# Kernel tuning notes

Measured on AMD Instinct MI355X. Metric: run time of the kernel, lower is better.

## Reference

```python
import jax, jax.numpy as jnp
import numpy as np

N_NODES = 100000
N_EDGES = 1600000
D_IN = 128
D_HID = 128
N_LAYERS = 3


def setup_inputs() -> dict:
    key = jax.random.key(0)
    k1, k2, k3, k4 = jax.random.split(key, 4)
    x = jax.random.normal(k1, (N_NODES, D_IN), dtype=jnp.float32)
    edge_index = jax.random.randint(k2, (2, N_EDGES), 0, N_NODES, dtype=jnp.int64)
    # Glorot-ish scale for stability across 3 layers
    Ws = jax.random.normal(k3, (N_LAYERS, D_IN, D_HID), dtype=jnp.float32) * (1.0 / np.sqrt(D_IN))
    bs = jax.random.normal(k4, (N_LAYERS, D_HID), dtype=jnp.float32) * 0.01
    return {"x": x, "edge_index": edge_index, "Ws": Ws, "bs": bs}


def _gcn_conv(x, row, col, deg_inv_sqrt, W, b, n_nodes):
    # Linear transform first (PyG GCNConv), then gather-normalize-scatter.
    h = x @ W                                        # [N, D]
    norm = deg_inv_sqrt[row] * deg_inv_sqrt[col]     # [E+N] (self-loops included)
    msg = h[row] * norm[:, None]                     # gather + scale, [E+N, D]
    out = jax.ops.segment_sum(msg, col, num_segments=n_nodes)  # scatter-add
    return out + b


def reference(x, edge_index, Ws, bs):
    n = x.shape[0]
    # add self-loops once (same for every layer)
    loop = jnp.arange(n, dtype=edge_index.dtype)
    row = jnp.concatenate([edge_index[0], loop])
    col = jnp.concatenate([edge_index[1], loop])
    # symmetric normalization: deg over target nodes (incl. self-loops)
    deg = jax.ops.segment_sum(jnp.ones_like(col, dtype=x.dtype), col, num_segments=n)
    deg_inv_sqrt = jnp.where(deg > 0, jax.lax.rsqrt(jnp.maximum(deg, 1.0)), 0.0)
    h = x
    for i in range(Ws.shape[0]):
        h = jax.nn.relu(_gcn_conv(h, row, col, deg_inv_sqrt, Ws[i], bs[i], n))
    return h
```

## Files before the change

kernel.cpp:

```cpp
#include <hip/hip_runtime.h>
#include <hip/hip_bf16.h>

#define NN 100000
#define NE 1600000
#define DD 128
#define NBUK 196
#define F1_BLOCKS 256
#define F3_BLOCKS 256

typedef unsigned short ushort_t;
typedef unsigned int uint_t;
typedef __attribute__((ext_vector_type(8))) short bf16x8;
typedef __attribute__((ext_vector_type(4))) float f32x4;

__device__ __forceinline__ ushort_t bf16rne(float f) {
    uint_t u = __float_as_uint(f);
    u += 0x7FFF + ((u >> 16) & 1);
    return (ushort_t)(u >> 16);
}
__device__ __forceinline__ float bfLo(uint_t u) { return __uint_as_float(u << 16); }
__device__ __forceinline__ float bfHi(uint_t u) { return __uint_as_float(u & 0xFFFF0000u); }


__global__ __launch_bounds__(256) void f1_bucket_count(const int* __restrict__ col,
                                                       int* __restrict__ bukCount) {
    __shared__ int hist[NBUK];
    for (int t = threadIdx.x; t < NBUK; t += 256) hist[t] = 0;
    __syncthreads();
    const int epb = (NE + F1_BLOCKS - 1) / F1_BLOCKS;
    const int e0 = blockIdx.x * epb;
    const int e1 = min(e0 + epb, NE);
    for (int e = e0 + threadIdx.x; e < e1; e += 256)
        atomicAdd(&hist[col[e] >> 9], 1);
    __syncthreads();
    for (int t = threadIdx.x; t < NBUK; t += 256)
        if (hist[t]) atomicAdd(&bukCount[t], hist[t]);
}

__global__ void f2_bucket_scan(const int* __restrict__ bukCount,
                               int* __restrict__ bukBase,
                               int* __restrict__ bukCursor,
                               int* __restrict__ offsets) {
    __shared__ int s[256];
    const int t = threadIdx.x;
    int v = (t < NBUK) ? bukCount[t] : 0;
    s[t] = v;
    __syncthreads();
    for (int off = 1; off < 256; off <<= 1) {
        int tmp = (t >= off) ? s[t - off] : 0;
        __syncthreads();
        s[t] += tmp;
        __syncthreads();
    }
    int excl = s[t] - v;
    if (t < NBUK) { bukBase[t] = excl; bukCursor[t] = excl; }
    if (t == 255) { bukBase[NBUK] = s[255]; offsets[NN] = s[255]; }
}

__global__ __launch_bounds__(256) void f3_scatter(const int* __restrict__ row,
                                                  const int* __restrict__ col,
                                                  int* __restrict__ bukCursor,
                                                  int* __restrict__ ebuf) {
    __shared__ int hist[4][NBUK];
    __shared__ int base[4][NBUK];
    const int t = threadIdx.x;
    const int w = t >> 6;
    const int lane = t & 63;
    for (int i = t; i < 4 * NBUK; i += 256) (&hist[0][0])[i] = 0;
    __syncthreads();
    const int epb = (NE + F3_BLOCKS - 1) / F3_BLOCKS;
    const int e0 = blockIdx.x * epb;
    const int e1 = min(e0 + epb, NE);
    const int wepb = (e1 - e0 + 3) >> 2;
    const int we0 = e0 + w * wepb;
    const int we1 = min(we0 + wepb, e1);
    for (int e = we0 + lane; e < we1; e += 64)
        atomicAdd(&hist[w][col[e] >> 9], 1);
    __syncthreads();
    if (t < NBUK) {
        int h0 = hist[0][t], h1 = hist[1][t], h2 = hist[2][t], h3 = hist[3][t];
        int tot = h0 + h1 + h2 + h3;
        int g = tot ? atomicAdd(&bukCursor[t], tot) : 0;
        base[0][t] = g; base[1][t] = g + h0;
        base[2][t] = g + h0 + h1; base[3][t] = g + h0 + h1 + h2;
        hist[0][t] = 0; hist[1][t] = 0; hist[2][t] = 0; hist[3][t] = 0;
    }
    __syncthreads();
    for (int e = we0 + lane; e < we1; e += 64) {
        int c = col[e];
        int b = c >> 9;
        int r = atomicAdd(&hist[w][b], 1);
        ebuf[base[w][b] + r] = (row[e] << 9) | (c & 511);
    }
}

__global__ __launch_bounds__(256) void f4_finalize(const int* __restrict__ ebuf,
                                                   const int* __restrict__ bukBase,
                                                   int* __restrict__ offsets,
                                                   float* __restrict__ dis,
                                                   int* __restrict__ csr_src) {
    __shared__ int cnt[512];
    __shared__ int cur[512];
    __shared__ int s[256];
    const int t = threadIdx.x;
    const int colBase = blockIdx.x << 9;
    const int ncols = min(512, NN - colBase);
    cnt[t] = 0; cnt[t + 256] = 0;
    __syncthreads();
    const int eb0 = bukBase[blockIdx.x];
    const int eb1 = bukBase[blockIdx.x + 1];
    for (int e = eb0 + t; e < eb1; e += 256)
        atomicAdd(&cnt[ebuf[e] & 511], 1);
    __syncthreads();
    const int c0 = cnt[2 * t], c1 = cnt[2 * t + 1];
    const int psum = c0 + c1;
    s[t] = psum;
    __syncthreads();
    for (int off = 1; off < 256; off <<= 1) {
        int tmp = (t >= off) ? s[t - off] : 0;
        __syncthreads();
        s[t] += tmp;
        __syncthreads();
    }
    const int exclPair = s[t] - psum;
    const int g0 = eb0 + exclPair;
    const int g1 = g0 + c0;
    cur[2 * t] = g0; cur[2 * t + 1] = g1;
    if (2 * t < ncols)     { offsets[colBase + 2 * t]     = g0; dis[colBase + 2 * t]     = rsqrtf((float)(c0 + 1)); }
    if (2 * t + 1 < ncols) { offsets[colBase + 2 * t + 1] = g1; dis[colBase + 2 * t + 1] = rsqrtf((float)(c1 + 1)); }
    __syncthreads();
    for (int e = eb0 + t; e < eb1; e += 256) {
        int pc = ebuf[e];
        int p = atomicAdd(&cur[pc & 511], 1);
        csr_src[p] = pc >> 9;
    }
}


__global__ __launch_bounds__(256) void wt_kernel(const float* __restrict__ Ws,
                                                 ushort_t* __restrict__ wT) {
    int idx = blockIdx.x * 256 + threadIdx.x;
    if (idx >= 3 * 128 * 16) return;
    int l = idx >> 11;
    int r = idx & 2047;
    int c = r >> 4;
    int kc = r & 15;
    const float* w = Ws + l * 16384;
    ushort_t tmp[8];
#pragma unroll
    for (int e = 0; e < 8; ++e)
        tmp[e] = bf16rne(w[(kc * 8 + e) * 128 + c]);
    *(uint4*)&wT[(size_t)l * 16384 + c * 128 + kc * 8] = *(uint4*)tmp;
}


template<bool XF32>
__global__ __launch_bounds__(256) void gemm_mfma(const void* __restrict__ Xv,
                                                 const ushort_t* __restrict__ wT,
                                                 const float* __restrict__ dis,
                                                 ushort_t* __restrict__ Y) {
    __shared__ short wlds[128 * 136];
    {
        const uint4* src = (const uint4*)wT;
        int t = threadIdx.x;
#pragma unroll
        for (int i = 0; i < 8; ++i) {
            int idx = i * 256 + t;
            int rowc = idx >> 4;
            int kc = idx & 15;
            uint4 v = src[idx];
            *(uint4*)&wlds[rowc * 136 + kc * 8] = v;
        }
    }
    __syncthreads();

    const int wave = threadIdx.x >> 6;
    const int lane = threadIdx.x & 63;
    const int m = lane & 15;
    const int kg = lane >> 4;
    const int r0 = blockIdx.x * 64 + wave * 16;
    const int rowA = min(r0 + m, NN - 1);

    f32x4 acc[8];
#pragma unroll
    for (int ct = 0; ct < 8; ++ct) acc[ct] = (f32x4){0.f, 0.f, 0.f, 0.f};

#pragma unroll
    for (int ks = 0; ks < 4; ++ks) {
        bf16x8 af;
        if (XF32) {
            const float* xp = (const float*)Xv + (size_t)rowA * DD + ks * 32 + kg * 8;
            float4 f0 = *(const float4*)xp;
            float4 f1 = *(const float4*)(xp + 4);
            af[0] = (short)bf16rne(f0.x); af[1] = (short)bf16rne(f0.y);
            af[2] = (short)bf16rne(f0.z); af[3] = (short)bf16rne(f0.w);
            af[4] = (short)bf16rne(f1.x); af[5] = (short)bf16rne(f1.y);
            af[6] = (short)bf16rne(f1.z); af[7] = (short)bf16rne(f1.w);
        } else {
            const ushort_t* xp = (const ushort_t*)Xv + (size_t)rowA * DD + ks * 32 + kg * 8;
            af = *(const bf16x8*)xp;
        }
#pragma unroll
        for (int ct = 0; ct < 8; ++ct) {
            bf16x8 bf = *(const bf16x8*)&wlds[(ct * 16 + m) * 136 + ks * 32 + kg * 8];
            acc[ct] = __builtin_amdgcn_mfma_f32_16x16x32_bf16(af, bf, acc[ct], 0, 0, 0);
        }
    }

    const int rbase = r0 + kg * 4;
    float dv[4];
#pragma unroll
    for (int rg = 0; rg < 4; ++rg) dv[rg] = dis[min(rbase + rg, NN - 1)];
#pragma unroll
    for (int ct = 0; ct < 8; ++ct) {
#pragma unroll
        for (int rg = 0; rg < 4; ++rg) {
            int row = rbase + rg;
            if (row < NN)
                Y[(size_t)row * DD + ct * 16 + m] = bf16rne(acc[ct][rg] * dv[rg]);
        }
    }
}


template<bool F32OUT>
__global__ __launch_bounds__(256) void agg_kernel(const uint_t* __restrict__ lin2,
                                                  const int* __restrict__ offsets,
                                                  const int* __restrict__ csr_src,
                                                  const float* __restrict__ dis,
                                                  const float* __restrict__ bias,
                                                  void* __restrict__ outv) {
    const int bid = blockIdx.x;
    const int xcd = bid & 7;
    const int h   = (xcd >> 2);
    const int g   = (bid >> 3) * 4 + (xcd & 3);
    const int w    = threadIdx.x >> 6;
    const int lane = threadIdx.x & 63;
    const int l32  = lane & 31;
    const int hi   = lane >> 5;
    const int v = g * 8 + w * 2 + hi;

    const int start = offsets[v];
    const int end   = offsets[v + 1];
    const int n     = end - start;
    const int nvm   = n < 32 ? n : 32;

    int idxv = 0;
    if (l32 < nvm) idxv = csr_src[start + l32];

    const int nv_other = __shfl(nvm, lane ^ 32);
    const int kmax = nvm > nv_other ? nvm : nv_other;

    const int doff = h * 32 + l32;
    const float dv = dis[v];
    uint_t self = lin2[(size_t)v * 64 + doff];
    float2 b    = ((const float2*)bias)[doff];

    float accx = 0.f, accy = 0.f;
    const int sbase = (lane & 32);
    for (int k = 0; k < kmax; k += 8) {
        int s0 = __shfl(idxv, sbase + k + 0);
        int s1 = __shfl(idxv, sbase + k + 1);
        int s2 = __shfl(idxv, sbase + k + 2);
        int s3 = __shfl(idxv, sbase + k + 3);
        int s4 = __shfl(idxv, sbase + k + 4);
        int s5 = __shfl(idxv, sbase + k + 5);
        int s6 = __shfl(idxv, sbase + k + 6);
        int s7 = __shfl(idxv, sbase + k + 7);
        uint_t a0 = lin2[(size_t)s0 * 64 + doff];
        uint_t a1 = lin2[(size_t)s1 * 64 + doff];
        uint_t a2 = lin2[(size_t)s2 * 64 + doff];
        uint_t a3 = lin2[(size_t)s3 * 64 + doff];
        uint_t a4 = lin2[(size_t)s4 * 64 + doff];
        uint_t a5 = lin2[(size_t)s5 * 64 + doff];
        uint_t a6 = lin2[(size_t)s6 * 64 + doff];
        uint_t a7 = lin2[(size_t)s7 * 64 + doff];
        if (k + 0 < nvm) { accx += bfLo(a0); accy += bfHi(a0); }
        if (k + 1 < nvm) { accx += bfLo(a1); accy += bfHi(a1); }
        if (k + 2 < nvm) { accx += bfLo(a2); accy += bfHi(a2); }
        if (k + 3 < nvm) { accx += bfLo(a3); accy += bfHi(a3); }
        if (k + 4 < nvm) { accx += bfLo(a4); accy += bfHi(a4); }
        if (k + 5 < nvm) { accx += bfLo(a5); accy += bfHi(a5); }
        if (k + 6 < nvm) { accx += bfLo(a6); accy += bfHi(a6); }
        if (k + 7 < nvm) { accx += bfLo(a7); accy += bfHi(a7); }
    }
    for (int e = start + 32; e < end; ++e) {
        int s = csr_src[e];
        uint_t a = lin2[(size_t)s * 64 + doff];
        accx += bfLo(a); accy += bfHi(a);
    }

    float rx = fmaxf(dv * (accx + bfLo(self)) + b.x, 0.f);
    float ry = fmaxf(dv * (accy + bfHi(self)) + b.y, 0.f);
    const size_t oidx = (size_t)v * 64 + doff;
    if (F32OUT) {
        float2 o = make_float2(rx, ry);
        __builtin_nontemporal_store(*(const double*)&o, (double*)((float2*)outv + oidx));
    } else {
        uint_t pk = (uint_t)bf16rne(rx) | ((uint_t)bf16rne(ry) << 16);
        __builtin_nontemporal_store(pk, (uint_t*)outv + oidx);
    }
}


extern "C" void kernel_launch(void* const* d_in, const int* in_sizes, int n_in,
                              void* d_out, int out_size, void* d_ws, size_t ws_size,
                              hipStream_t stream) {
    const float* x   = (const float*)d_in[0];
    const int*   ei  = (const int*)d_in[1];
    const float* Ws  = (const float*)d_in[2];
    const float* bs  = (const float*)d_in[3];

    const int* row = ei;
    const int* col = ei + NE;

    char* ws = (char*)d_ws;
    ushort_t* lin    = (ushort_t*)(ws + 0);
    int*   ebuf      = (int*)  (ws + 0);
    ushort_t* hb     = (ushort_t*)(ws + 25600000);
    float* dis       = (float*)(ws + 51200000);
    int*   offsets   = (int*)  (ws + 51600000);
    int*   csr_src   = (int*)  (ws + 52000016);
    int*   bukCount  = (int*)  (ws + 58400016);
    int*   bukBase   = (int*)  (ws + 58400800);
    int*   bukCursor = (int*)  (ws + 58401600);
    ushort_t* wT     = (ushort_t*)(ws + 58402432);

    hipMemsetAsync(bukCount, 0, NBUK * sizeof(int), stream);
    f1_bucket_count<<<F1_BLOCKS, 256, 0, stream>>>(col, bukCount);
    f2_bucket_scan<<<1, 256, 0, stream>>>(bukCount, bukBase, bukCursor, offsets);
    f3_scatter<<<F3_BLOCKS, 256, 0, stream>>>(row, col, bukCursor, ebuf);
    f4_finalize<<<NBUK, 256, 0, stream>>>(ebuf, bukBase, offsets, dis, csr_src);
    wt_kernel<<<24, 256, 0, stream>>>(Ws, wT);

    const int gemmGrid = (NN + 63) / 64;
    const int aggGrid = (NN / 8) * 2;
    gemm_mfma<true><<<gemmGrid, 256, 0, stream>>>(x, wT, dis, lin);
    agg_kernel<false><<<aggGrid, 256, 0, stream>>>((const uint_t*)lin, offsets, csr_src, dis, bs, hb);
    gemm_mfma<false><<<gemmGrid, 256, 0, stream>>>(hb, wT + 16384, dis, lin);
    agg_kernel<false><<<aggGrid, 256, 0, stream>>>((const uint_t*)lin, offsets, csr_src, dis, bs + DD, hb);
    gemm_mfma<false><<<gemmGrid, 256, 0, stream>>>(hb, wT + 32768, dis, lin);
    agg_kernel<true><<<aggGrid, 256, 0, stream>>>((const uint_t*)lin, offsets, csr_src, dis, bs + 2 * DD, d_out);
}
```

Before: 291.9 us.

## Stage GEMM output through LDS for coalesced stores and pad rows for branchless gather

The GEMM epilogue now writes bf16 results into shared memory and then stores each row with 16-byte vector stores, where before it issued scattered 2-byte stores. The output buffer is padded to 100032 rows, with zero rows written past N. The aggregation kernel points unused neighbor slots at the zero row NN, so the unrolled gather needs no per-element predicates. It also rounds the loop count up to a multiple of 8 and uses 32-bit shift/or indexing. The cost is an extra barrier and LDS round trip in the GEMM, plus a few redundant loads of the padding row.

New measurement: 293.2 us. Within noise of the previous version (+0.5%).

```diff
diff --git a/kernel.cpp b/kernel.cpp
--- a/kernel.cpp
+++ b/kernel.cpp
@@ -2,6 +2,7 @@
 #include <hip/hip_bf16.h>
 
 #define NN 100000
+#define NROWS 100032
 #define NE 1600000
 #define DD 128
 #define NBUK 196
@@ -159,7 +160,7 @@
                                                  const ushort_t* __restrict__ wT,
                                                  const float* __restrict__ dis,
                                                  ushort_t* __restrict__ Y) {
-    __shared__ short wlds[128 * 136];
+    __shared__ short smem[128 * 136];
     {
         const uint4* src = (const uint4*)wT;
         int t = threadIdx.x;
@@ -169,7 +170,7 @@
             int rowc = idx >> 4;
             int kc = idx & 15;
             uint4 v = src[idx];
-            *(uint4*)&wlds[rowc * 136 + kc * 8] = v;
+            *(uint4*)&smem[rowc * 136 + kc * 8] = v;
         }
     }
     __syncthreads();
@@ -202,11 +203,14 @@
         }
 #pragma unroll
         for (int ct = 0; ct < 8; ++ct) {
-            bf16x8 bf = *(const bf16x8*)&wlds[(ct * 16 + m) * 136 + ks * 32 + kg * 8];
+            bf16x8 bf = *(const bf16x8*)&smem[(ct * 16 + m) * 136 + ks * 32 + kg * 8];
             acc[ct] = __builtin_amdgcn_mfma_f32_16x16x32_bf16(af, bf, acc[ct], 0, 0, 0);
         }
     }
 
+    __syncthreads();
+
+    ushort_t* sl = (ushort_t*)smem;
     const int rbase = r0 + kg * 4;
     float dv[4];
 #pragma unroll
@@ -214,12 +218,29 @@
 #pragma unroll
     for (int ct = 0; ct < 8; ++ct) {
 #pragma unroll
-        for (int rg = 0; rg < 4; ++rg) {
-            int row = rbase + rg;
-            if (row < NN)
-                Y[(size_t)row * DD + ct * 16 + m] = bf16rne(acc[ct][rg] * dv[rg]);
-        }
-    }
+        for (int rg = 0; rg < 4; ++rg)
+            sl[(wave * 16 + kg * 4 + rg) * 132 + ct * 16 + m] = bf16rne(acc[ct][rg] * dv[rg]);
+    }
+
+    const int lr = lane >> 2;
+    const int q  = lane & 3;
+    const int grow = r0 + lr;
+    const ushort_t* rb = sl + (wave * 16 + lr) * 132 + q * 32;
+    uint2 d0 = *(const uint2*)(rb + 0);
+    uint2 d1 = *(const uint2*)(rb + 4);
+    uint2 d2 = *(const uint2*)(rb + 8);
+    uint2 d3 = *(const uint2*)(rb + 12);
+    uint2 d4 = *(const uint2*)(rb + 16);
+    uint2 d5 = *(const uint2*)(rb + 20);
+    uint2 d6 = *(const uint2*)(rb + 24);
+    uint2 d7 = *(const uint2*)(rb + 28);
+    const bool ok = grow < NN;
+    uint4 v0 = ok ? make_uint4(d0.x, d0.y, d1.x, d1.y) : make_uint4(0, 0, 0, 0);
+    uint4 v1 = ok ? make_uint4(d2.x, d2.y, d3.x, d3.y) : make_uint4(0, 0, 0, 0);
+    uint4 v2 = ok ? make_uint4(d4.x, d4.y, d5.x, d5.y) : make_uint4(0, 0, 0, 0);
+    uint4 v3 = ok ? make_uint4(d6.x, d6.y, d7.x, d7.y) : make_uint4(0, 0, 0, 0);
+    uint4* yp = (uint4*)&Y[(size_t)grow * DD + q * 32];
+    yp[0] = v0; yp[1] = v1; yp[2] = v2; yp[3] = v3;
 }
 
 
@@ -245,15 +266,16 @@
     const int n     = end - start;
     const int nvm   = n < 32 ? n : 32;
 
-    int idxv = 0;
+    int idxv = NN;
     if (l32 < nvm) idxv = csr_src[start + l32];
 
     const int nv_other = __shfl(nvm, lane ^ 32);
-    const int kmax = nvm > nv_other ? nvm : nv_other;
-
-    const int doff = h * 32 + l32;
+    int kmax = nvm > nv_other ? nvm : nv_other;
+    kmax = (kmax + 7) & ~7;
+
+    const uint_t doff = (uint_t)(h * 32 + l32);
     const float dv = dis[v];
-    uint_t self = lin2[(size_t)v * 64 + doff];
+    uint_t self = lin2[((uint_t)v << 6) | doff];
     float2 b    = ((const float2*)bias)[doff];
 
     float accx = 0.f, accy = 0.f;
@@ -267,26 +289,22 @@
         int s5 = __shfl(idxv, sbase + k + 5);
         int s6 = __shfl(idxv, sbase + k + 6);
         int s7 = __shfl(idxv, sbase + k + 7);
-        uint_t a0 = lin2[(size_t)s0 * 64 + doff];
-        uint_t a1 = lin2[(size_t)s1 * 64 + doff];
-        uint_t a2 = lin2[(size_t)s2 * 64 + doff];
-        uint_t a3 = lin2[(size_t)s3 * 64 + doff];
-        uint_t a4 = lin2[(size_t)s4 * 64 + doff];
-        uint_t a5 = lin2[(size_t)s5 * 64 + doff];
-        uint_t a6 = lin2[(size_t)s6 * 64 + doff];
-        uint_t a7 = lin2[(size_t)s7 * 64 + doff];
-        if (k + 0 < nvm) { accx += bfLo(a0); accy += bfHi(a0); }
-        if (k + 1 < nvm) { accx += bfLo(a1); accy += bfHi(a1); }
-        if (k + 2 < nvm) { accx += bfLo(a2); accy += bfHi(a2); }
-        if (k + 3 < nvm) { accx += bfLo(a3); accy += bfHi(a3); }
-        if (k + 4 < nvm) { accx += bfLo(a4); accy += bfHi(a4); }
-        if (k + 5 < nvm) { accx += bfLo(a5); accy += bfHi(a5); }
-        if (k + 6 < nvm) { accx += bfLo(a6); accy += bfHi(a6); }
-        if (k + 7 < nvm) { accx += bfLo(a7); accy += bfHi(a7); }
+        uint_t a0 = lin2[((uint_t)s0 << 6) | doff];
+        uint_t a1 = lin2[((uint_t)s1 << 6) | doff];
+        uint_t a2 = lin2[((uint_t)s2 << 6) | doff];
+        uint_t a3 = lin2[((uint_t)s3 << 6) | doff];
+        uint_t a4 = lin2[((uint_t)s4 << 6) | doff];
+        uint_t a5 = lin2[((uint_t)s5 << 6) | doff];
+        uint_t a6 = lin2[((uint_t)s6 << 6) | doff];
+        uint_t a7 = lin2[((uint_t)s7 << 6) | doff];
+        accx += bfLo(a0) + bfLo(a1) + bfLo(a2) + bfLo(a3)
+              + bfLo(a4) + bfLo(a5) + bfLo(a6) + bfLo(a7);
+        accy += bfHi(a0) + bfHi(a1) + bfHi(a2) + bfHi(a3)
+              + bfHi(a4) + bfHi(a5) + bfHi(a6) + bfHi(a7);
     }
     for (int e = start + 32; e < end; ++e) {
-        int s = csr_src[e];
-        uint_t a = lin2[(size_t)s * 64 + doff];
+        uint_t s = (uint_t)csr_src[e];
+        uint_t a = lin2[(s << 6) | doff];
         accx += bfLo(a); accy += bfHi(a);
     }
 
@@ -317,14 +335,14 @@
     char* ws = (char*)d_ws;
     ushort_t* lin    = (ushort_t*)(ws + 0);
     int*   ebuf      = (int*)  (ws + 0);
-    ushort_t* hb     = (ushort_t*)(ws + 25600000);
-    float* dis       = (float*)(ws + 51200000);
-    int*   offsets   = (int*)  (ws + 51600000);
-    int*   csr_src   = (int*)  (ws + 52000016);
-    int*   bukCount  = (int*)  (ws + 58400016);
-    int*   bukBase   = (int*)  (ws + 58400800);
-    int*   bukCursor = (int*)  (ws + 58401600);
-    ushort_t* wT     = (ushort_t*)(ws + 58402432);
+    ushort_t* hb     = (ushort_t*)(ws + 25608192);
+    float* dis       = (float*)(ws + 51208192);
+    int*   offsets   = (int*)  (ws + 51608192);
+    int*   csr_src   = (int*)  (ws + 52008208);
+    int*   bukCount  = (int*)  (ws + 58408208);
+    int*   bukBase   = (int*)  (ws + 58409008);
+    int*   bukCursor = (int*)  (ws + 58409808);
+    ushort_t* wT     = (ushort_t*)(ws + 58410608);
 
     hipMemsetAsync(bukCount, 0, NBUK * sizeof(int), stream);
     f1_bucket_count<<<F1_BLOCKS, 256, 0, stream>>>(col, bukCount);
@@ -333,7 +351,7 @@
     f4_finalize<<<NBUK, 256, 0, stream>>>(ebuf, bukBase, offsets, dis, csr_src);
     wt_kernel<<<24, 256, 0, stream>>>(Ws, wT);
 
-    const int gemmGrid = (NN + 63) / 64;
+    const int gemmGrid = NROWS / 64;
     const int aggGrid = (NN / 8) * 2;
     gemm_mfma<true><<<gemmGrid, 256, 0, stream>>>(x, wT, dis, lin);
     agg_kernel<false><<<aggGrid, 256, 0, stream>>>((const uint_t*)lin, offsets, csr_src, dis, bs, hb);
```
